# Kernel optimization log

Measured on AMD Instinct MI355X. Metric: run time of the kernel, lower is better.

## Reference

```python
import jax, jax.numpy as jnp
import numpy as np

E = 1024      # embed_dim (== embed_dim_)
NH = 8        # num_heads
HD = E // NH  # head_dim
BS1 = 2048
BS2 = 2048
EPS = 1e-5


def _layernorm(x, g, b):
    m = jnp.mean(x, axis=-1, keepdims=True)
    v = jnp.mean(jnp.square(x - m), axis=-1, keepdims=True)
    return (x - m) * jax.lax.rsqrt(v + EPS) * g + b


def setup_inputs() -> dict:
    key = jax.random.key(0)
    ks = jax.random.split(key, 16)
    s = 1.0 / np.sqrt(E)
    s4 = 1.0 / np.sqrt(4 * E)
    inp = {
        "x1": jax.random.normal(ks[0], (BS1, E), jnp.float32),
        "x2": jax.random.normal(ks[1], (BS2, E), jnp.float32),
        "Wq": jax.random.uniform(ks[2], (E, E), jnp.float32, -s, s),
        "bq": jax.random.uniform(ks[3], (E,), jnp.float32, -s, s),
        "Wk": jax.random.uniform(ks[4], (E, E), jnp.float32, -s, s),
        "bk": jax.random.uniform(ks[5], (E,), jnp.float32, -s, s),
        "Wv": jax.random.uniform(ks[6], (E, E), jnp.float32, -s, s),
        "bv": jax.random.uniform(ks[7], (E,), jnp.float32, -s, s),
        "Wo": jax.random.uniform(ks[8], (E, E), jnp.float32, -s, s),
        "bo": jax.random.uniform(ks[9], (E,), jnp.float32, -s, s),
        "W1": jax.random.uniform(ks[10], (4 * E, E), jnp.float32, -s, s),
        "b1": jax.random.uniform(ks[11], (4 * E,), jnp.float32, -s, s),
        "W2": jax.random.uniform(ks[12], (E, 4 * E), jnp.float32, -s4, s4),
        "b2": jax.random.uniform(ks[13], (E,), jnp.float32, -s4, s4),
        "g1": jnp.ones((E,), jnp.float32),
        "be1": jnp.zeros((E,), jnp.float32),
        "g2": jnp.ones((E,), jnp.float32),
        "be2": jnp.zeros((E,), jnp.float32),
    }
    return inp


def reference(x1, x2, Wq, bq, Wk, bk, Wv, bv, Wo, bo, W1, b1, W2, b2, g1, be1, g2, be2):
    scale = HD ** -0.5
    # Projections; attention runs over the batch axis (n=bs1, m=bs2)
    q = (x1 @ Wq.T + bq).reshape(BS1, NH, HD)   # [n,h,d]
    k = (x2 @ Wk.T + bk).reshape(BS2, NH, HD)   # [m,h,d]
    v = (x2 @ Wv.T + bv).reshape(BS2, NH, HD)   # [m,h,d]
    scores = jnp.einsum('nhd,mhd->nmh', q, k) * scale  # [n,m,h]
    # NOTE: faithful to source: softmax over the HEADS axis (dim=-1)
    probs = jax.nn.softmax(scores, axis=-1)
    # dropout is identity in eval mode
    attn = jnp.einsum('nmh,mhd->nhd', probs, v).reshape(BS1, E)
    attn = attn @ Wo.T + bo
    h = _layernorm(x1 + attn, g1, be1)
    ffn = jax.nn.relu(h @ W1.T + b1) @ W2.T + b2
    return _layernorm(h + ffn, g2, be2)
```

## Files before the change

kernel.cpp:

```cpp
#include <hip/hip_runtime.h>

#define BS 2048
#define EMB 1024
#define NHEAD 8
#define HDIM 128

typedef unsigned short u16;
typedef __attribute__((ext_vector_type(8))) short bf16x8;
typedef __attribute__((ext_vector_type(4))) float f32x4;

__device__ __forceinline__ u16 f32_bf16(float f) {
  unsigned u = __float_as_uint(f);
  u += 0x7fffu + ((u >> 16) & 1u);
  return (u16)(u >> 16);
}
__device__ __forceinline__ float bf2f(u16 x) {
  return __uint_as_float((unsigned)x << 16);
}

__device__ __forceinline__ void gld_lds16(const void* g, void* l) {
  __builtin_amdgcn_global_load_lds(
      (const __attribute__((address_space(1))) void*)g,
      (__attribute__((address_space(3))) void*)l, 16, 0, 0);
}

struct CvtArgs { const float* src[8]; };
__global__ __launch_bounds__(256) void cvt_all(CvtArgs a, u16* __restrict__ dst) {
  long i = (long)blockIdx.x * 256 + threadIdx.x;
  int seg = (int)(i >> 18);
  const float* src; long b;
  if (seg < 2)       { src = a.src[0]; b = 0; }
  else if (seg < 4)  { src = a.src[1]; b = 2L << 18; }
  else if (seg == 4) { src = a.src[2]; b = 4L << 18; }
  else if (seg == 5) { src = a.src[3]; b = 5L << 18; }
  else if (seg == 6) { src = a.src[4]; b = 6L << 18; }
  else if (seg == 7) { src = a.src[5]; b = 7L << 18; }
  else if (seg < 12) { src = a.src[6]; b = 8L << 18; }
  else               { src = a.src[7]; b = 12L << 18; }
  float4 v = ((const float4*)src)[i - b];
  ushort4 o;
  o.x = f32_bf16(v.x); o.y = f32_bf16(v.y); o.z = f32_bf16(v.z); o.w = f32_bf16(v.w);
  ((ushort4*)dst)[i] = o;
}

__device__ __forceinline__ void gemm_core(
    const u16* __restrict__ A, const u16* __restrict__ B, void* __restrict__ Cp,
    const float* __restrict__ bias, int K, int lda, int ldb, int ldc,
    long cbase, int mode, int relu, int m0, int n0) {
  __shared__ __align__(16) u16 As[128 * 32];
  __shared__ __align__(16) u16 Bs[128 * 32];
  const int t = threadIdx.x;
  const int lane = t & 63, l15 = lane & 15, quad = lane >> 4;
  const int wv = t >> 6, wr = wv & 1, wc = wv >> 1;
  const int wbase = t & ~63;

  f32x4 acc[4][4];
#pragma unroll
  for (int r = 0; r < 4; ++r)
#pragma unroll
    for (int c = 0; c < 4; ++c) acc[r][c] = (f32x4){0.f, 0.f, 0.f, 0.f};

  for (int k0 = 0; k0 < K; k0 += 32) {
#pragma unroll
    for (int i = 0; i < 2; ++i) {
      int s = i * 256 + t;
      gld_lds16(A + (long)(m0 + (s >> 2)) * lda + k0 + (s & 3) * 8,
                As + (i * 256 + wbase) * 8);
    }
#pragma unroll
    for (int i = 0; i < 2; ++i) {
      int s = i * 256 + t;
      gld_lds16(B + (long)(n0 + (s >> 2)) * ldb + k0 + (s & 3) * 8,
                Bs + (i * 256 + wbase) * 8);
    }
    __syncthreads();
    bf16x8 fa[4], fb[4];
#pragma unroll
    for (int r = 0; r < 4; ++r)
      fa[r] = *(const bf16x8*)&As[(wr * 64 + r * 16 + l15) * 32 + quad * 8];
#pragma unroll
    for (int c = 0; c < 4; ++c)
      fb[c] = *(const bf16x8*)&Bs[(wc * 64 + c * 16 + l15) * 32 + quad * 8];
#pragma unroll
    for (int r = 0; r < 4; ++r)
#pragma unroll
      for (int c = 0; c < 4; ++c)
        acc[r][c] = __builtin_amdgcn_mfma_f32_16x16x32_bf16(fa[r], fb[c], acc[r][c], 0, 0, 0);
    __syncthreads();
  }

#pragma unroll
  for (int r = 0; r < 4; ++r)
#pragma unroll
    for (int c = 0; c < 4; ++c) {
      const int m = m0 + wr * 64 + r * 16 + quad * 4;
      const int n = n0 + wc * 64 + c * 16 + l15;
      const float bv = bias ? bias[n] : 0.f;
      f32x4 v = acc[r][c];
      if (mode == 2) {
        ushort4 o;
        o.x = f32_bf16(v[0] + bv);
        o.y = f32_bf16(v[1] + bv);
        o.z = f32_bf16(v[2] + bv);
        o.w = f32_bf16(v[3] + bv);
        *(ushort4*)((u16*)Cp + cbase + (long)n * ldc + m) = o;
      } else {
#pragma unroll
        for (int i = 0; i < 4; ++i) {
          float x = v[i] + bv;
          if (relu) x = fmaxf(x, 0.f);
          if (mode == 0)
            ((float*)Cp)[cbase + (long)(m + i) * ldc + n] = x;
          else
            ((u16*)Cp)[cbase + (long)(m + i) * ldc + n] = f32_bf16(x);
        }
      }
    }
}

__global__ __launch_bounds__(256) void gemm_bt_k(
    const u16* __restrict__ A, const u16* __restrict__ B, void* __restrict__ C,
    const float* __restrict__ bias, int K, int lda, int ldb, int ldc,
    long aOffZ, long bOffZ, long cOffZ, int mode, int relu) {
  gemm_core(A + (long)blockIdx.z * aOffZ, B + (long)blockIdx.z * bOffZ, C, bias,
            K, lda, ldb, ldc, (long)blockIdx.z * cOffZ, mode, relu,
            blockIdx.y * 128, blockIdx.x * 128);
}

__global__ __launch_bounds__(256) void qkv_kernel(
    const u16* __restrict__ x1b, const u16* __restrict__ x2b,
    const u16* __restrict__ Wqb, const u16* __restrict__ Wkb, const u16* __restrict__ Wvb,
    const float* __restrict__ bq, const float* __restrict__ bk, const float* __restrict__ bv,
    u16* __restrict__ Qb, u16* __restrict__ Kb, u16* __restrict__ Vt) {
  const int z = blockIdx.z;
  const u16* A = (z == 0) ? x1b : x2b;
  const u16* B = (z == 0) ? Wqb : (z == 1) ? Wkb : Wvb;
  void* C = (z == 0) ? (void*)Qb : (z == 1) ? (void*)Kb : (void*)Vt;
  const float* bias = (z == 0) ? bq : (z == 1) ? bk : bv;
  const int mode = (z == 2) ? 2 : 1;
  const int ldc = (z == 2) ? 2048 : 1024;
  gemm_core(A, B, C, bias, 1024, 1024, 1024, ldc, 0, mode, 0,
            blockIdx.y * 128, blockIdx.x * 128);
}

__global__ __launch_bounds__(256) void pv_kernel(
    const u16* __restrict__ P, const u16* __restrict__ Vt, u16* __restrict__ parts) {
  const int h = blockIdx.z >> 1, ks = blockIdx.z & 1;
  const u16* A = P + (long)h * BS * BS + ks * 1024;
  const u16* B = Vt + (long)h * HDIM * 2048 + ks * 1024;
  const long cbase = (long)ks * BS * 1024 + h * HDIM;
  gemm_core(A, B, parts, nullptr, 1024, 2048, 2048, 1024, cbase, 1, 0,
            blockIdx.y * 128, 0);
}

__global__ __launch_bounds__(256) void reduce2_bf16(
    const u16* __restrict__ p0, const u16* __restrict__ p1, u16* __restrict__ out) {
  int i = blockIdx.x * 256 + threadIdx.x;
  ushort4 a = ((const ushort4*)p0)[i];
  ushort4 b = ((const ushort4*)p1)[i];
  ushort4 o;
  o.x = f32_bf16(bf2f(a.x) + bf2f(b.x));
  o.y = f32_bf16(bf2f(a.y) + bf2f(b.y));
  o.z = f32_bf16(bf2f(a.z) + bf2f(b.z));
  o.w = f32_bf16(bf2f(a.w) + bf2f(b.w));
  ((ushort4*)out)[i] = o;
}

__global__ __launch_bounds__(256) void scores_softmax(
    const u16* __restrict__ Q, const u16* __restrict__ Km, u16* __restrict__ P) {
  __shared__ __align__(16) u16 Qs[32 * 128];
  __shared__ __align__(16) u16 Ks[128 * 128];
  const int t = threadIdx.x;
  const int lane = t & 63, l15 = lane & 15, quad = lane >> 4;
  const int wv = t >> 6;
  const int n0 = blockIdx.y * 32, m0 = blockIdx.x * 128;
  const int wbase = t & ~63;

  f32x4 acc[8][2][2];
#pragma unroll
  for (int h = 0; h < 8; ++h)
#pragma unroll
    for (int r = 0; r < 2; ++r)
#pragma unroll
      for (int c = 0; c < 2; ++c) acc[h][r][c] = (f32x4){0.f, 0.f, 0.f, 0.f};

#pragma unroll
  for (int h = 0; h < 8; ++h) {
#pragma unroll
    for (int i = 0; i < 2; ++i) {
      int s = i * 256 + t;
      gld_lds16(Q + (long)(n0 + ((s >> 2) & 31)) * EMB + h * HDIM + (s >> 7) * 32 + (s & 3) * 8,
                Qs + (i * 256 + wbase) * 8);
    }
#pragma unroll
    for (int i = 0; i < 8; ++i) {
      int s = i * 256 + t;
      gld_lds16(Km + (long)(m0 + ((s >> 2) & 127)) * EMB + h * HDIM + (s >> 9) * 32 + (s & 3) * 8,
                Ks + (i * 256 + wbase) * 8);
    }
    __syncthreads();
#pragma unroll
    for (int kk = 0; kk < 4; ++kk) {
      bf16x8 fa[2], fb[2];
#pragma unroll
      for (int r = 0; r < 2; ++r)
        fa[r] = *(const bf16x8*)&Qs[kk * 1024 + (r * 16 + l15) * 32 + quad * 8];
#pragma unroll
      for (int c = 0; c < 2; ++c)
        fb[c] = *(const bf16x8*)&Ks[kk * 4096 + (wv * 32 + c * 16 + l15) * 32 + quad * 8];
#pragma unroll
      for (int r = 0; r < 2; ++r)
#pragma unroll
        for (int c = 0; c < 2; ++c)
          acc[h][r][c] = __builtin_amdgcn_mfma_f32_16x16x32_bf16(fa[r], fb[c], acc[h][r][c], 0, 0, 0);
    }
    __syncthreads();
  }

  const float scale = 0.08838834764831845f;
#pragma unroll
  for (int r = 0; r < 2; ++r)
#pragma unroll
    for (int c = 0; c < 2; ++c)
#pragma unroll
      for (int i = 0; i < 4; ++i) {
        float mx = acc[0][r][c][i];
#pragma unroll
        for (int h = 1; h < 8; ++h) mx = fmaxf(mx, acc[h][r][c][i]);
        float sum = 0.f;
#pragma unroll
        for (int h = 0; h < 8; ++h) {
          float e = __expf((acc[h][r][c][i] - mx) * scale);
          acc[h][r][c][i] = e;
          sum += e;
        }
        float inv = 1.f / sum;
#pragma unroll
        for (int h = 0; h < 8; ++h) acc[h][r][c][i] *= inv;
      }

#pragma unroll
  for (int h = 0; h < 8; ++h) {
#pragma unroll
    for (int r = 0; r < 2; ++r)
#pragma unroll
      for (int c = 0; c < 2; ++c)
#pragma unroll
        for (int i = 0; i < 4; ++i) {
          int nl = r * 16 + quad * 4 + i;
          int ml = (wv * 32 + c * 16 + l15) ^ (quad << 3);
          Qs[nl * 128 + ml] = f32_bf16(acc[h][r][c][i]);
        }
    __syncthreads();
#pragma unroll
    for (int j = 0; j < 2; ++j) {
      int ch = j * 256 + t;
      int row = ch >> 4;
      int col = (ch & 15) * 8;
      int sw = ((row >> 2) & 3) << 3;
      uint4 val = *(const uint4*)&Qs[row * 128 + (col ^ sw)];
      *(uint4*)&P[(long)h * BS * BS + (long)(n0 + row) * BS + m0 + col] = val;
    }
    __syncthreads();
  }
}

__global__ __launch_bounds__(256) void ln_residual3(
    const float* __restrict__ x, const float* __restrict__ y0, const float* __restrict__ y1,
    const float* __restrict__ colb, const float* __restrict__ g, const float* __restrict__ b,
    float* __restrict__ out32, u16* __restrict__ out16) {
  const int row = blockIdx.x, t = threadIdx.x;
  float4 v = ((const float4*)(x + (long)row * EMB))[t];
  float4 u0 = ((const float4*)(y0 + (long)row * EMB))[t];
  float4 u1 = ((const float4*)(y1 + (long)row * EMB))[t];
  float4 cb = ((const float4*)colb)[t];
  v.x += u0.x + u1.x + cb.x;
  v.y += u0.y + u1.y + cb.y;
  v.z += u0.z + u1.z + cb.z;
  v.w += u0.w + u1.w + cb.w;
  float s = v.x + v.y + v.z + v.w;
  float q = v.x * v.x + v.y * v.y + v.z * v.z + v.w * v.w;
#pragma unroll
  for (int off = 32; off > 0; off >>= 1) {
    s += __shfl_xor(s, off);
    q += __shfl_xor(q, off);
  }
  __shared__ float red[8];
  const int wv = t >> 6, lane = t & 63;
  if (lane == 0) { red[wv] = s; red[4 + wv] = q; }
  __syncthreads();
  s = red[0] + red[1] + red[2] + red[3];
  q = red[4] + red[5] + red[6] + red[7];
  const float mean = s * (1.f / EMB);
  const float var = q * (1.f / EMB) - mean * mean;
  const float rstd = rsqrtf(var + 1e-5f);
  float4 gg = ((const float4*)g)[t];
  float4 bb = ((const float4*)b)[t];
  float4 o;
  o.x = (v.x - mean) * rstd * gg.x + bb.x;
  o.y = (v.y - mean) * rstd * gg.y + bb.y;
  o.z = (v.z - mean) * rstd * gg.z + bb.z;
  o.w = (v.w - mean) * rstd * gg.w + bb.w;
  ((float4*)(out32 + (long)row * EMB))[t] = o;
  if (out16) {
    ushort4 ho;
    ho.x = f32_bf16(o.x); ho.y = f32_bf16(o.y); ho.z = f32_bf16(o.z); ho.w = f32_bf16(o.w);
    ((ushort4*)(out16 + (long)row * EMB))[t] = ho;
  }
}

extern "C" void kernel_launch(void* const* d_in, const int* in_sizes, int n_in,
                              void* d_out, int out_size, void* d_ws, size_t ws_size,
                              hipStream_t stream) {
  const float* x1 = (const float*)d_in[0];
  const float* x2 = (const float*)d_in[1];
  const float* Wq = (const float*)d_in[2];
  const float* bq = (const float*)d_in[3];
  const float* Wk = (const float*)d_in[4];
  const float* bk = (const float*)d_in[5];
  const float* Wv = (const float*)d_in[6];
  const float* bv = (const float*)d_in[7];
  const float* Wo = (const float*)d_in[8];
  const float* bo = (const float*)d_in[9];
  const float* W1 = (const float*)d_in[10];
  const float* b1 = (const float*)d_in[11];
  const float* W2 = (const float*)d_in[12];
  const float* b2 = (const float*)d_in[13];
  const float* g1 = (const float*)d_in[14];
  const float* be1 = (const float*)d_in[15];
  const float* g2 = (const float*)d_in[16];
  const float* be2 = (const float*)d_in[17];

  char* ws = (char*)d_ws;
  const size_t MB = 1ull << 20;
  u16* x1b = (u16*)(ws + 0 * MB);
  u16* x2b = (u16*)(ws + 4 * MB);
  u16* Wqb = (u16*)(ws + 8 * MB);
  u16* Wkb = (u16*)(ws + 10 * MB);
  u16* Wvb = (u16*)(ws + 12 * MB);
  u16* Wob = (u16*)(ws + 14 * MB);
  u16* W1b = (u16*)(ws + 16 * MB);
  u16* W2b = (u16*)(ws + 24 * MB);
  u16* Qb  = (u16*)(ws + 32 * MB);
  u16* Kb  = (u16*)(ws + 36 * MB);
  u16* pvP0 = Qb;
  u16* pvP1 = Kb;
  u16* Vtb = (u16*)(ws + 40 * MB);
  u16* attnb = (u16*)(ws + 44 * MB);
  u16* P   = (u16*)(ws + 48 * MB);
  float* woP0 = (float*)(ws + 48 * MB);
  float* woP1 = (float*)(ws + 56 * MB);
  float* h32  = (float*)(ws + 64 * MB);
  u16*  h16   = (u16*)(ws + 72 * MB);
  u16*  ffn1b = (u16*)(ws + 76 * MB);
  float* f2P0 = woP0;
  float* f2P1 = woP1;

  CvtArgs ca;
  ca.src[0] = x1; ca.src[1] = x2; ca.src[2] = Wq; ca.src[3] = Wk;
  ca.src[4] = Wv; ca.src[5] = Wo; ca.src[6] = W1; ca.src[7] = W2;
  cvt_all<<<16384, 256, 0, stream>>>(ca, (u16*)ws);

  qkv_kernel<<<dim3(8, 16, 3), 256, 0, stream>>>(x1b, x2b, Wqb, Wkb, Wvb, bq, bk, bv, Qb, Kb, Vtb);

  scores_softmax<<<dim3(16, 64, 1), 256, 0, stream>>>(Qb, Kb, P);

  pv_kernel<<<dim3(1, 16, 16), 256, 0, stream>>>(P, Vtb, pvP0);

  reduce2_bf16<<<2048, 256, 0, stream>>>(pvP0, pvP1, attnb);

  gemm_bt_k<<<dim3(8, 16, 2), 256, 0, stream>>>(attnb, Wob, woP0, nullptr,
                                                512, 1024, 1024, 1024,
                                                512, 512, (long)BS * 1024, 0, 0);

  ln_residual3<<<2048, 256, 0, stream>>>(x1, woP0, woP1, bo, g1, be1, h32, h16);

  gemm_bt_k<<<dim3(32, 16, 1), 256, 0, stream>>>(h16, W1b, ffn1b, b1,
                                                 1024, 1024, 1024, 4096,
                                                 0, 0, 0, 1, 1);

  gemm_bt_k<<<dim3(8, 16, 2), 256, 0, stream>>>(ffn1b, W2b, f2P0, nullptr,
                                                2048, 4096, 4096, 1024,
                                                2048, 2048, (long)BS * 1024, 0, 0);

  ln_residual3<<<2048, 256, 0, stream>>>(h32, f2P0, f2P1, b2, g2, be2, (float*)d_out, nullptr);
}
```

Before: 352.1 us.

## Fuse scores, head-softmax and PV into one attention kernel with split-M partials

Replaces the separate scores+softmax kernel (which wrote a 64 MB bf16 probability tensor P) and the PV GEMM with a single fused kernel. Each block keeps the probabilities in LDS and accumulates O for all 8 heads in registers, and it double-buffers the Q/K/V tile loads. The M dimension is split into 4 chunks whose bf16 partial outputs are summed by a new 4-way reduce kernel. This removes the large P write and read from HBM, but it needs high register pressure (two 8x2x2 f32x4 accumulator sets), about 1 block per CU, and only 256 blocks in the grid.

```diff
diff --git a/kernel.cpp b/kernel.cpp
--- a/kernel.cpp
+++ b/kernel.cpp
@@ -143,126 +143,176 @@
             blockIdx.y * 128, blockIdx.x * 128);
 }
 
-__global__ __launch_bounds__(256) void pv_kernel(
-    const u16* __restrict__ P, const u16* __restrict__ Vt, u16* __restrict__ parts) {
-  const int h = blockIdx.z >> 1, ks = blockIdx.z & 1;
-  const u16* A = P + (long)h * BS * BS + ks * 1024;
-  const u16* B = Vt + (long)h * HDIM * 2048 + ks * 1024;
-  const long cbase = (long)ks * BS * 1024 + h * HDIM;
-  gemm_core(A, B, parts, nullptr, 1024, 2048, 2048, 1024, cbase, 1, 0,
-            blockIdx.y * 128, 0);
-}
-
-__global__ __launch_bounds__(256) void reduce2_bf16(
-    const u16* __restrict__ p0, const u16* __restrict__ p1, u16* __restrict__ out) {
-  int i = blockIdx.x * 256 + threadIdx.x;
-  ushort4 a = ((const ushort4*)p0)[i];
-  ushort4 b = ((const ushort4*)p1)[i];
-  ushort4 o;
-  o.x = f32_bf16(bf2f(a.x) + bf2f(b.x));
-  o.y = f32_bf16(bf2f(a.y) + bf2f(b.y));
-  o.z = f32_bf16(bf2f(a.z) + bf2f(b.z));
-  o.w = f32_bf16(bf2f(a.w) + bf2f(b.w));
-  ((ushort4*)out)[i] = o;
-}
-
-__global__ __launch_bounds__(256) void scores_softmax(
-    const u16* __restrict__ Q, const u16* __restrict__ Km, u16* __restrict__ P) {
-  __shared__ __align__(16) u16 Qs[32 * 128];
-  __shared__ __align__(16) u16 Ks[128 * 128];
+__global__ __launch_bounds__(256, 1) void fused_attn(
+    const u16* __restrict__ Qg, const u16* __restrict__ Kg,
+    const u16* __restrict__ Vt, u16* __restrict__ parts) {
+  __shared__ __align__(16) u16 Qs[2][4096];
+  __shared__ __align__(16) u16 Ks[2][16384];
+  __shared__ __align__(16) u16 Vs[2][16384];
+  __shared__ __align__(16) u16 Ps[4096];
   const int t = threadIdx.x;
   const int lane = t & 63, l15 = lane & 15, quad = lane >> 4;
-  const int wv = t >> 6;
-  const int n0 = blockIdx.y * 32, m0 = blockIdx.x * 128;
-  const int wbase = t & ~63;
-
-  f32x4 acc[8][2][2];
-#pragma unroll
-  for (int h = 0; h < 8; ++h)
-#pragma unroll
-    for (int r = 0; r < 2; ++r)
-#pragma unroll
-      for (int c = 0; c < 2; ++c) acc[h][r][c] = (f32x4){0.f, 0.f, 0.f, 0.f};
-
-#pragma unroll
-  for (int h = 0; h < 8; ++h) {
+  const int wv = t >> 6, wbase = t & ~63;
+  const int chunk = blockIdx.x;
+  const int n0 = blockIdx.y * 32;
+
+  auto stageQ = [&](int h, int b) {
 #pragma unroll
     for (int i = 0; i < 2; ++i) {
       int s = i * 256 + t;
-      gld_lds16(Q + (long)(n0 + ((s >> 2) & 31)) * EMB + h * HDIM + (s >> 7) * 32 + (s & 3) * 8,
-                Qs + (i * 256 + wbase) * 8);
-    }
+      gld_lds16(Qg + (long)(n0 + ((s >> 2) & 31)) * EMB + h * HDIM + (s >> 7) * 32 + (s & 3) * 8,
+                &Qs[b][(i * 256 + wbase) * 8]);
+    }
+  };
+  auto stageK = [&](int h, int b, int m0) {
 #pragma unroll
     for (int i = 0; i < 8; ++i) {
       int s = i * 256 + t;
-      gld_lds16(Km + (long)(m0 + ((s >> 2) & 127)) * EMB + h * HDIM + (s >> 9) * 32 + (s & 3) * 8,
-                Ks + (i * 256 + wbase) * 8);
-    }
-    __syncthreads();
-#pragma unroll
-    for (int kk = 0; kk < 4; ++kk) {
-      bf16x8 fa[2], fb[2];
+      gld_lds16(Kg + (long)(m0 + ((s >> 2) & 127)) * EMB + h * HDIM + (s >> 9) * 32 + (s & 3) * 8,
+                &Ks[b][(i * 256 + wbase) * 8]);
+    }
+  };
+  auto stageV = [&](int h, int b, int m0) {
+#pragma unroll
+    for (int i = 0; i < 8; ++i) {
+      int s = i * 256 + t;
+      gld_lds16(Vt + (long)(h * HDIM + ((s >> 2) & 127)) * 2048 + m0 + (s >> 9) * 32 + (s & 3) * 8,
+                &Vs[b][(i * 256 + wbase) * 8]);
+    }
+  };
+
+  f32x4 O[8][2][2];
+#pragma unroll
+  for (int h = 0; h < 8; ++h)
+#pragma unroll
+    for (int r = 0; r < 2; ++r)
+#pragma unroll
+      for (int c = 0; c < 2; ++c) O[h][r][c] = (f32x4){0.f, 0.f, 0.f, 0.f};
+
+  stageQ(0, 0);
+  stageK(0, 0, chunk * 512);
+
+  for (int mt = 0; mt < 4; ++mt) {
+    const int m0 = chunk * 512 + mt * 128;
+    f32x4 acc[8][2][2];
+#pragma unroll
+    for (int h = 0; h < 8; ++h)
 #pragma unroll
       for (int r = 0; r < 2; ++r)
-        fa[r] = *(const bf16x8*)&Qs[kk * 1024 + (r * 16 + l15) * 32 + quad * 8];
+#pragma unroll
+        for (int c = 0; c < 2; ++c) acc[h][r][c] = (f32x4){0.f, 0.f, 0.f, 0.f};
+
+#pragma unroll
+    for (int h = 0; h < 8; ++h) {
+      __syncthreads();
+      if (h < 7) { stageQ(h + 1, (h + 1) & 1); stageK(h + 1, (h + 1) & 1, m0); }
+      const u16* qb = Qs[h & 1];
+      const u16* kb = Ks[h & 1];
+#pragma unroll
+      for (int kk = 0; kk < 4; ++kk) {
+        bf16x8 fa[2], fb[2];
+#pragma unroll
+        for (int r = 0; r < 2; ++r)
+          fa[r] = *(const bf16x8*)&qb[kk * 1024 + (r * 16 + l15) * 32 + quad * 8];
+#pragma unroll
+        for (int c = 0; c < 2; ++c)
+          fb[c] = *(const bf16x8*)&kb[kk * 4096 + (wv * 32 + c * 16 + l15) * 32 + quad * 8];
+#pragma unroll
+        for (int r = 0; r < 2; ++r)
+#pragma unroll
+          for (int c = 0; c < 2; ++c)
+            acc[h][r][c] = __builtin_amdgcn_mfma_f32_16x16x32_bf16(fa[r], fb[c], acc[h][r][c], 0, 0, 0);
+      }
+    }
+
+    stageV(0, 0, m0);
+
+    const float scale = 0.08838834764831845f;
+#pragma unroll
+    for (int r = 0; r < 2; ++r)
 #pragma unroll
       for (int c = 0; c < 2; ++c)
-        fb[c] = *(const bf16x8*)&Ks[kk * 4096 + (wv * 32 + c * 16 + l15) * 32 + quad * 8];
+#pragma unroll
+        for (int i = 0; i < 4; ++i) {
+          float mx = acc[0][r][c][i];
+#pragma unroll
+          for (int h = 1; h < 8; ++h) mx = fmaxf(mx, acc[h][r][c][i]);
+          float sum = 0.f;
+#pragma unroll
+          for (int h = 0; h < 8; ++h) {
+            float e = __expf((acc[h][r][c][i] - mx) * scale);
+            acc[h][r][c][i] = e;
+            sum += e;
+          }
+          float inv = 1.f / sum;
+#pragma unroll
+          for (int h = 0; h < 8; ++h) acc[h][r][c][i] *= inv;
+        }
+
+#pragma unroll
+    for (int h = 0; h < 8; ++h) {
+      __syncthreads();
 #pragma unroll
       for (int r = 0; r < 2; ++r)
 #pragma unroll
         for (int c = 0; c < 2; ++c)
-          acc[h][r][c] = __builtin_amdgcn_mfma_f32_16x16x32_bf16(fa[r], fb[c], acc[h][r][c], 0, 0, 0);
-    }
-    __syncthreads();
+#pragma unroll
+          for (int i = 0; i < 4; ++i) {
+            int n = r * 16 + quad * 4 + i;
+            int e = (c * 16 + l15) ^ (quad << 3);
+            Ps[wv * 1024 + n * 32 + e] = f32_bf16(acc[h][r][c][i]);
+          }
+      __syncthreads();
+      if (h < 7) stageV(h + 1, (h + 1) & 1, m0);
+      if (h == 0 && mt < 3) { stageQ(0, 0); stageK(0, 0, m0 + 128); }
+      const u16* vb = Vs[h & 1];
+#pragma unroll
+      for (int kk = 0; kk < 4; ++kk) {
+        bf16x8 fa[2], fb[2];
+#pragma unroll
+        for (int rr = 0; rr < 2; ++rr)
+          fa[rr] = *(const bf16x8*)&Ps[kk * 1024 + (rr * 16 + l15) * 32 +
+                                       (((quad ^ (l15 >> 2)) & 3) << 3)];
+#pragma unroll
+        for (int c = 0; c < 2; ++c)
+          fb[c] = *(const bf16x8*)&vb[kk * 4096 + (wv * 32 + c * 16 + l15) * 32 + quad * 8];
+#pragma unroll
+        for (int rr = 0; rr < 2; ++rr)
+#pragma unroll
+          for (int c = 0; c < 2; ++c)
+            O[h][rr][c] = __builtin_amdgcn_mfma_f32_16x16x32_bf16(fa[rr], fb[c], O[h][rr][c], 0, 0, 0);
+      }
+    }
   }
 
-  const float scale = 0.08838834764831845f;
-#pragma unroll
-  for (int r = 0; r < 2; ++r)
-#pragma unroll
-    for (int c = 0; c < 2; ++c)
-#pragma unroll
-      for (int i = 0; i < 4; ++i) {
-        float mx = acc[0][r][c][i];
-#pragma unroll
-        for (int h = 1; h < 8; ++h) mx = fmaxf(mx, acc[h][r][c][i]);
-        float sum = 0.f;
-#pragma unroll
-        for (int h = 0; h < 8; ++h) {
-          float e = __expf((acc[h][r][c][i] - mx) * scale);
-          acc[h][r][c][i] = e;
-          sum += e;
+#pragma unroll
+  for (int h = 0; h < 8; ++h)
+#pragma unroll
+    for (int r = 0; r < 2; ++r)
+#pragma unroll
+      for (int c = 0; c < 2; ++c)
+#pragma unroll
+        for (int i = 0; i < 4; ++i) {
+          int n = n0 + r * 16 + quad * 4 + i;
+          int col = h * HDIM + wv * 32 + c * 16 + l15;
+          parts[(long)chunk * BS * EMB + (long)n * EMB + col] = f32_bf16(O[h][r][c][i]);
         }
-        float inv = 1.f / sum;
-#pragma unroll
-        for (int h = 0; h < 8; ++h) acc[h][r][c][i] *= inv;
-      }
-
-#pragma unroll
-  for (int h = 0; h < 8; ++h) {
-#pragma unroll
-    for (int r = 0; r < 2; ++r)
-#pragma unroll
-      for (int c = 0; c < 2; ++c)
-#pragma unroll
-        for (int i = 0; i < 4; ++i) {
-          int nl = r * 16 + quad * 4 + i;
-          int ml = (wv * 32 + c * 16 + l15) ^ (quad << 3);
-          Qs[nl * 128 + ml] = f32_bf16(acc[h][r][c][i]);
-        }
-    __syncthreads();
-#pragma unroll
-    for (int j = 0; j < 2; ++j) {
-      int ch = j * 256 + t;
-      int row = ch >> 4;
-      int col = (ch & 15) * 8;
-      int sw = ((row >> 2) & 3) << 3;
-      uint4 val = *(const uint4*)&Qs[row * 128 + (col ^ sw)];
-      *(uint4*)&P[(long)h * BS * BS + (long)(n0 + row) * BS + m0 + col] = val;
-    }
-    __syncthreads();
-  }
+}
+
+__global__ __launch_bounds__(256) void reduce4_bf16(
+    const u16* __restrict__ p, u16* __restrict__ out) {
+  long i = (long)blockIdx.x * 256 + threadIdx.x;
+  const long S = (long)BS * EMB / 4;
+  ushort4 a0 = ((const ushort4*)p)[i];
+  ushort4 a1 = ((const ushort4*)p)[i + S];
+  ushort4 a2 = ((const ushort4*)p)[i + 2 * S];
+  ushort4 a3 = ((const ushort4*)p)[i + 3 * S];
+  ushort4 o;
+  o.x = f32_bf16(bf2f(a0.x) + bf2f(a1.x) + bf2f(a2.x) + bf2f(a3.x));
+  o.y = f32_bf16(bf2f(a0.y) + bf2f(a1.y) + bf2f(a2.y) + bf2f(a3.y));
+  o.z = f32_bf16(bf2f(a0.z) + bf2f(a1.z) + bf2f(a2.z) + bf2f(a3.z));
+  o.w = f32_bf16(bf2f(a0.w) + bf2f(a1.w) + bf2f(a2.w) + bf2f(a3.w));
+  ((ushort4*)out)[i] = o;
 }
 
 __global__ __launch_bounds__(256) void ln_residual3(
@@ -343,16 +393,14 @@
   u16* W2b = (u16*)(ws + 24 * MB);
   u16* Qb  = (u16*)(ws + 32 * MB);
   u16* Kb  = (u16*)(ws + 36 * MB);
-  u16* pvP0 = Qb;
-  u16* pvP1 = Kb;
   u16* Vtb = (u16*)(ws + 40 * MB);
   u16* attnb = (u16*)(ws + 44 * MB);
-  u16* P   = (u16*)(ws + 48 * MB);
-  float* woP0 = (float*)(ws + 48 * MB);
-  float* woP1 = (float*)(ws + 56 * MB);
-  float* h32  = (float*)(ws + 64 * MB);
-  u16*  h16   = (u16*)(ws + 72 * MB);
-  u16*  ffn1b = (u16*)(ws + 76 * MB);
+  u16* Oparts = (u16*)(ws + 48 * MB);
+  float* woP0 = (float*)(ws + 64 * MB);
+  float* woP1 = (float*)(ws + 72 * MB);
+  float* h32  = (float*)(ws + 80 * MB);
+  u16*  h16   = (u16*)(ws + 88 * MB);
+  u16*  ffn1b = (u16*)(ws + 92 * MB);
   float* f2P0 = woP0;
   float* f2P1 = woP1;
 
@@ -363,11 +411,9 @@
 
   qkv_kernel<<<dim3(8, 16, 3), 256, 0, stream>>>(x1b, x2b, Wqb, Wkb, Wvb, bq, bk, bv, Qb, Kb, Vtb);
 
-  scores_softmax<<<dim3(16, 64, 1), 256, 0, stream>>>(Qb, Kb, P);
-
-  pv_kernel<<<dim3(1, 16, 16), 256, 0, stream>>>(P, Vtb, pvP0);
-
-  reduce2_bf16<<<2048, 256, 0, stream>>>(pvP0, pvP1, attnb);
+  fused_attn<<<dim3(4, 64), 256, 0, stream>>>(Qb, Kb, Vtb, Oparts);
+
+  reduce4_bf16<<<2048, 256, 0, stream>>>(Oparts, attnb);
 
   gemm_bt_k<<<dim3(8, 16, 2), 256, 0, stream>>>(attnb, Wob, woP0, nullptr,
                                                 512, 1024, 1024, 1024,
```

Result: slower. 366.5 us (+4.1%).
